# Performance work log

Hardware: AMD Instinct MI355X
Metric: run time of the kernel (lower is better)

Reference implementation:

```python
import jax, jax.numpy as jnp
import numpy as np

B, FH, N, TIN = 8, 8, 2048, 5      # batch(time for LSTM), f_length, nodes, in_length
H1, H2 = 32, 64                    # traj_linear_hidden, lstm_encoder_size
NEG = -9e15

def setup_inputs() -> dict:
    key = jax.random.key(0)
    ks = jax.random.split(key, 12)
    s = lambda k, shape, fan: jax.random.normal(k, shape, jnp.float32) * (1.0 / np.sqrt(fan))
    return {
        "hist": jax.random.normal(ks[0], (B, FH, N, TIN), jnp.float32),
        "adj": jax.random.randint(ks[1], (B, 2, N, N), 0, 2, jnp.int32),
        "W1": s(ks[2], (H1, TIN * FH), TIN * FH),
        "b1": jnp.zeros((H1,), jnp.float32),
        "W_ih": s(ks[3], (4 * H2, H1), H1),
        "W_hh": s(ks[4], (4 * H2, H2), H2),
        "b_ih": jnp.zeros((4 * H2,), jnp.float32),
        "b_hh": jnp.zeros((4 * H2,), jnp.float32),
        "Wg": s(ks[5], (H2, H2), H2),
        "a_src": s(ks[6], (H2,), H2),
        "a_dst": s(ks[7], (H2,), H2),
    }

def _lstm(x, W_ih, W_hh, b_ih, b_hh):
    # x: [T, Nb, H1] (torch nn.LSTM seq-first); gate order i,f,g,o
    Nb = x.shape[1]
    h0 = jnp.zeros((Nb, H2), x.dtype)
    c0 = jnp.zeros((Nb, H2), x.dtype)
    def step(carry, xt):
        h, c = carry
        g = xt @ W_ih.T + b_ih + h @ W_hh.T + b_hh        # [Nb, 4*H2]
        i, f, gg, o = jnp.split(g, 4, axis=-1)
        c = jax.nn.sigmoid(f) * c + jax.nn.sigmoid(i) * jnp.tanh(gg)
        h = jax.nn.sigmoid(o) * jnp.tanh(c)
        return (h, c), h
    _, hs = jax.lax.scan(step, (h0, c0), x)
    return hs                                              # [T, Nb, H2]

def reference(hist, adj, W1, b1, W_ih, W_hh, b_ih, b_hh, Wg, a_src, a_dst):
    # hist.permute(0,2,3,1).flatten(2,3) -> [B, N, TIN*FH]
    x = jnp.transpose(hist, (0, 2, 3, 1)).reshape(B, N, TIN * FH)
    h1 = jax.nn.elu(x @ W1.T + b1)                         # [B, N, H1]
    hs = _lstm(h1, W_ih, W_hh, b_ih, b_hh)                 # [B, N, H2]
    # GAT over adj[:, -1]
    A = adj[:, -1, :, :] > 0                               # [B, N, N]
    Wh = hs @ Wg                                           # [B, N, H2]
    e = jax.nn.leaky_relu(
        (Wh @ a_src)[:, :, None] + (Wh @ a_dst)[:, None, :], 0.2)
    e = jnp.where(A, e, NEG)
    alpha = jax.nn.softmax(e, axis=-1)                     # [B, N, N]
    out = jax.nn.elu(jnp.einsum("bij,bjd->bid", alpha, Wh))
    return out
```

## Files before the change

kernel.cpp:

```cpp
#include <hip/hip_runtime.h>
#include <hip/hip_bf16.h>
#include <math.h>

#define BB 8
#define FH 8
#define NN 2048
#define TIN 5
#define H1 32
#define H2 64

typedef const void* cvp;
typedef __attribute__((ext_vector_type(8))) short short8;
typedef __attribute__((ext_vector_type(4))) float floatx4;

__device__ __forceinline__ float ldx(cvp p, int i, int bf) {
  if (bf) return __bfloat162float(((const __hip_bfloat16*)p)[i]);
  return ((const float*)p)[i];
}

__device__ __forceinline__ float4 ld4(cvp p, int i, int bf) {
  if (bf) {
    const __hip_bfloat162* q = (const __hip_bfloat162*)p;
    float2 a = __bfloat1622float2(q[(i >> 1)]);
    float2 b = __bfloat1622float2(q[(i >> 1) + 1]);
    return make_float4(a.x, a.y, b.x, b.y);
  }
  return ((const float4*)p)[i >> 2];
}

__device__ __forceinline__ float sigf(float x) {
  return 1.f / (1.f + __expf(-x));
}

__device__ __forceinline__ int detect_bf(cvp wih) {
  unsigned word = ((const unsigned*)wih)[threadIdx.x & 63];
  unsigned e = (word >> 7) & 0xFFu;
  unsigned long long bal = __ballot(e >= 100u && e <= 150u);
  return __popcll(bal) > 44;
}

__global__ __launch_bounds__(256, 2) void k_lstm(
    cvp hist, cvp W1, cvp b1, cvp W_ih, cvp W_hh, cvp b_ih, cvp b_hh,
    cvp Wg, cvp a_src, cvp a_dst,
    __hip_bfloat16* __restrict__ WhFr, float* __restrict__ sv,
    float* __restrict__ dv) {
  __shared__ __align__(16) float xh[4][96];
  __shared__ float gbuf[4][256];
  __shared__ float W1s[H1][41];
  __shared__ float b1s[H1];
  __shared__ float xstage[4][40];
  int bf = detect_bf(W_ih);
  int tid = threadIdx.x;
  int w = tid >> 6, lane = tid & 63;
  int g = tid;
  int n0 = blockIdx.x << 2;
  int node_w = n0 + w;

  for (int i = tid; i < H1 * 40; i += 256) W1s[i / 40][i % 40] = ldx(W1, i, bf);
  if (tid < H1) b1s[tid] = ldx(b1, tid, bf);

  float wreg[96];
#pragma unroll
  for (int kq = 0; kq < 8; ++kq) {
    float4 v = ld4(W_ih, g * 32 + (kq << 2), bf);
    wreg[(kq << 2) + 0] = v.x; wreg[(kq << 2) + 1] = v.y;
    wreg[(kq << 2) + 2] = v.z; wreg[(kq << 2) + 3] = v.w;
  }
#pragma unroll
  for (int kq = 0; kq < 16; ++kq) {
    float4 v = ld4(W_hh, g * 64 + (kq << 2), bf);
    wreg[32 + (kq << 2) + 0] = v.x; wreg[32 + (kq << 2) + 1] = v.y;
    wreg[32 + (kq << 2) + 2] = v.z; wreg[32 + (kq << 2) + 3] = v.w;
  }
  float bias = ldx(b_ih, g, bf) + ldx(b_hh, g, bf);

  float wgreg[64];
#pragma unroll
  for (int k = 0; k < H2; ++k) wgreg[k] = ldx(Wg, (k << 6) + lane, bf);
  float as = ldx(a_src, lane, bf);
  float ad = ldx(a_dst, lane, bf);

  size_t o8base = ((size_t)(node_w >> 5) * 256) + ((size_t)(lane >> 4) * 64) +
                  (((node_w >> 3) & 3) * 16) + (lane & 15);
  int jj = node_w & 7;

  xh[w][32 + lane] = 0.f;
  float c = 0.f;

  for (int t = 0; t < BB; ++t) {
    if (tid < 160) {
      int nd = tid / 40, r = tid % 40;
      int ti = r >> 3, f = r & 7;
      xstage[nd][r] = ldx(hist, ((t * FH + f) * NN + n0 + nd) * TIN + ti, bf);
    }
    __syncthreads();
    if (tid < 128) {
      int nd = tid >> 5, k = tid & 31;
      float acc = b1s[k];
#pragma unroll
      for (int j = 0; j < 40; ++j) acc += W1s[k][j] * xstage[nd][j];
      xh[nd][k] = (acc > 0.f) ? acc : expm1f(acc);
    }
    __syncthreads();
    float acc[4] = {bias, bias, bias, bias};
    const float4* xq0 = (const float4*)xh[0];
    const float4* xq1 = (const float4*)xh[1];
    const float4* xq2 = (const float4*)xh[2];
    const float4* xq3 = (const float4*)xh[3];
#pragma unroll
    for (int kq = 0; kq < 24; ++kq) {
      float w0 = wreg[(kq << 2) + 0], w1 = wreg[(kq << 2) + 1];
      float w2 = wreg[(kq << 2) + 2], w3 = wreg[(kq << 2) + 3];
      float4 v0 = xq0[kq], v1 = xq1[kq], v2 = xq2[kq], v3 = xq3[kq];
      acc[0] += w0 * v0.x + w1 * v0.y + w2 * v0.z + w3 * v0.w;
      acc[1] += w0 * v1.x + w1 * v1.y + w2 * v1.z + w3 * v1.w;
      acc[2] += w0 * v2.x + w1 * v2.y + w2 * v2.z + w3 * v2.w;
      acc[3] += w0 * v3.x + w1 * v3.y + w2 * v3.z + w3 * v3.w;
    }
#pragma unroll
    for (int nd = 0; nd < 4; ++nd) gbuf[nd][g] = acc[nd];
    __syncthreads();
    float gi = gbuf[w][lane];
    float gf = gbuf[w][64 + lane];
    float gg = gbuf[w][128 + lane];
    float go = gbuf[w][192 + lane];
    c = sigf(gf) * c + sigf(gi) * tanhf(gg);
    float h = sigf(go) * tanhf(c);
    xh[w][32 + lane] = h;

    float wh = 0.f;
    const float4* hq = (const float4*)&xh[w][32];
#pragma unroll
    for (int kq = 0; kq < 16; ++kq) {
      float4 hv = hq[kq];
      wh += hv.x * wgreg[(kq << 2) + 0] + hv.y * wgreg[(kq << 2) + 1] +
            hv.z * wgreg[(kq << 2) + 2] + hv.w * wgreg[(kq << 2) + 3];
    }
    float s = wh * as, d = wh * ad;
#pragma unroll
    for (int off = 32; off > 0; off >>= 1) {
      s += __shfl_xor(s, off, 64);
      d += __shfl_xor(d, off, 64);
    }
    if (lane == 0) {
      sv[t * NN + node_w] = s;
      dv[t * NN + node_w] = d;
    }
    WhFr[((size_t)t * 16384 + o8base) * 8 + jj] = __float2bfloat16(wh);
    __syncthreads();
  }
}

__global__ __launch_bounds__(256, 4) void k_gat(
    const int* __restrict__ adj, const __hip_bfloat16* __restrict__ WhFr,
    const float* __restrict__ sv, const float* __restrict__ dv,
    void* __restrict__ out, cvp W_ih) {
  __shared__ __align__(16) float dv_s[NN];
  __shared__ unsigned int msk[16 * 65];
  __shared__ floatx4 abuf[3][5][64];
  int bf = detect_bf(W_ih);
  int tid = threadIdx.x;
  int w = tid >> 6, lane = tid & 63;
  int b = blockIdx.x >> 7;
  int i0 = (blockIdx.x & 127) << 4;
  int q = lane >> 4, m = lane & 15;

  for (int j = tid; j < 16 * 65; j += 256) msk[j] = 0u;
  for (int j = tid; j < NN; j += 256) dv_s[j] = dv[b * NN + j];
  float sva = sv[b * NN + i0 + m];
  __syncthreads();

  const int4* adj4 = (const int4*)(adj + ((size_t)(b * 2 + 1) * NN + i0) * NN);
#pragma unroll 16
  for (int gi = 0; gi < 32; ++gi) {
    int g = (w << 5) + gi;
    int row = g >> 3, seg = g & 7;
    int4 v = adj4[(size_t)row * 512 + (seg << 6) + lane];
    unsigned nib = (v.x != 0 ? 1u : 0u) | (v.y != 0 ? 2u : 0u) |
                   (v.z != 0 ? 4u : 0u) | (v.w != 0 ? 8u : 0u);
    atomicOr(&msk[row * 65 + (seg << 3) + (lane >> 3)], nib << ((lane & 7) << 2));
  }
  __syncthreads();

  short8 ones;
#pragma unroll
  for (int p = 0; p < 8; ++p) ones[p] = (short)0x3F80;

  const short8* base = ((const short8*)WhFr) + (size_t)b * 16384 + lane;
  int ksb = w << 4, kse = ksb + 16;
  floatx4 acc0 = {0.f, 0.f, 0.f, 0.f};
  floatx4 acc1 = acc0, acc2 = acc0, acc3 = acc0, accS = acc0;

  for (int ks = ksb; ks < kse; ++ks) {
    const short8* b_ks = base + (size_t)ks * 256;
    short8 b0 = b_ks[0];
    short8 b1 = b_ks[64];
    short8 b2 = b_ks[128];
    short8 b3 = b_ks[192];
    unsigned mword = msk[m * 65 + ks];
    float4 d0 = *(const float4*)&dv_s[(ks << 5) + (q << 3)];
    float4 d1 = *(const float4*)&dv_s[(ks << 5) + (q << 3) + 4];
    float dd[8] = {d0.x, d0.y, d0.z, d0.w, d1.x, d1.y, d1.z, d1.w};
    float pv[8];
#pragma unroll
    for (int jj = 0; jj < 8; ++jj) {
      float t = sva + dd[jj];
      float e = __expf(fmaxf(t, 0.2f * t));
      pv[jj] = ((mword >> ((q << 3) + jj)) & 1u) ? e : 0.f;
    }
    short8 afr;
#pragma unroll
    for (int p2 = 0; p2 < 4; ++p2)
      ((__hip_bfloat162*)&afr)[p2] =
          __float22bfloat162_rn(make_float2(pv[2 * p2], pv[2 * p2 + 1]));
    acc0 = __builtin_amdgcn_mfma_f32_16x16x32_bf16(afr, b0, acc0, 0, 0, 0);
    acc1 = __builtin_amdgcn_mfma_f32_16x16x32_bf16(afr, b1, acc1, 0, 0, 0);
    acc2 = __builtin_amdgcn_mfma_f32_16x16x32_bf16(afr, b2, acc2, 0, 0, 0);
    acc3 = __builtin_amdgcn_mfma_f32_16x16x32_bf16(afr, b3, acc3, 0, 0, 0);
    accS = __builtin_amdgcn_mfma_f32_16x16x32_bf16(afr, ones, accS, 0, 0, 0);
  }
  if (w > 0) {
    abuf[w - 1][0][lane] = acc0;
    abuf[w - 1][1][lane] = acc1;
    abuf[w - 1][2][lane] = acc2;
    abuf[w - 1][3][lane] = acc3;
    abuf[w - 1][4][lane] = accS;
  }
  __syncthreads();
  if (w != 0) return;
#pragma unroll
  for (int ww = 0; ww < 3; ++ww) {
    acc0 += abuf[ww][0][lane];
    acc1 += abuf[ww][1][lane];
    acc2 += abuf[ww][2][lane];
    acc3 += abuf[ww][3][lane];
    accS += abuf[ww][4][lane];
  }
  floatx4 accs[4] = {acc0, acc1, acc2, acc3};
  float inv[4];
#pragma unroll
  for (int r = 0; r < 4; ++r) inv[r] = 1.f / accS[r];
  if (bf) {
    __hip_bfloat16* o = (__hip_bfloat16*)out;
#pragma unroll
    for (int nt = 0; nt < 4; ++nt)
#pragma unroll
      for (int r = 0; r < 4; ++r) {
        float v = accs[nt][r] * inv[r];
        v = (v > 0.f) ? v : expm1f(v);
        int row = i0 + (q << 2) + r;
        o[((size_t)b * NN + row) * H2 + (nt << 4) + m] = __float2bfloat16(v);
      }
  } else {
    float* o = (float*)out;
#pragma unroll
    for (int nt = 0; nt < 4; ++nt)
#pragma unroll
      for (int r = 0; r < 4; ++r) {
        float v = accs[nt][r] * inv[r];
        v = (v > 0.f) ? v : expm1f(v);
        int row = i0 + (q << 2) + r;
        o[((size_t)b * NN + row) * H2 + (nt << 4) + m] = v;
      }
  }
}

extern "C" void kernel_launch(void* const* d_in, const int* in_sizes, int n_in,
                              void* d_out, int out_size, void* d_ws, size_t ws_size,
                              hipStream_t stream) {
  (void)in_sizes; (void)n_in; (void)out_size; (void)ws_size;
  cvp hist  = d_in[0];
  const int* adj = (const int*)d_in[1];
  cvp W1    = d_in[2];
  cvp b1    = d_in[3];
  cvp W_ih  = d_in[4];
  cvp W_hh  = d_in[5];
  cvp b_ih  = d_in[6];
  cvp b_hh  = d_in[7];
  cvp Wg    = d_in[8];
  cvp a_src = d_in[9];
  cvp a_dst = d_in[10];

  __hip_bfloat16* WhFr = (__hip_bfloat16*)d_ws;
  float* sv = (float*)d_ws + 524288;
  float* dv = sv + BB * NN;

  k_lstm<<<512, 256, 0, stream>>>(hist, W1, b1, W_ih, W_hh, b_ih, b_hh,
                                  Wg, a_src, a_dst, WhFr, sv, dv);
  k_gat<<<1024, 256, 0, stream>>>(adj, WhFr, sv, dv, d_out, W_ih);
}
```

Measured before the change: 398.4 us.

## Move adjacency bitmask packing into LSTM kernel to overlap with recurrence

Reading the 128MB int32 adjacency slice and packing it into bitmasks moves out of the GAT kernel and into the latency-bound LSTM kernel. There the loads are interleaved with each timestep's compute, and the result goes to a global bitmask in the workspace. The GAT kernel then loads only the packed mask plus vectorized dv. The goal is to hide the memory-bound adjacency scan behind the LSTM's sync-heavy recurrence. In exchange the LSTM kernel gains register pressure, LDS use and shared-memory atomics.

Result: faster. 381.9 us (-4.1%).

```diff
diff --git a/kernel.cpp b/kernel.cpp
--- a/kernel.cpp
+++ b/kernel.cpp
@@ -41,14 +41,15 @@
 
 __global__ __launch_bounds__(256, 2) void k_lstm(
     cvp hist, cvp W1, cvp b1, cvp W_ih, cvp W_hh, cvp b_ih, cvp b_hh,
-    cvp Wg, cvp a_src, cvp a_dst,
+    cvp Wg, cvp a_src, cvp a_dst, const int* __restrict__ adj,
     __hip_bfloat16* __restrict__ WhFr, float* __restrict__ sv,
-    float* __restrict__ dv) {
+    float* __restrict__ dv, unsigned* __restrict__ gmask) {
   __shared__ __align__(16) float xh[4][96];
   __shared__ float gbuf[4][256];
   __shared__ float W1s[H1][41];
   __shared__ float b1s[H1];
   __shared__ float xstage[4][40];
+  __shared__ __align__(16) unsigned pmsk[2048];
   int bf = detect_bf(W_ih);
   int tid = threadIdx.x;
   int w = tid >> 6, lane = tid & 63;
@@ -58,6 +59,11 @@
 
   for (int i = tid; i < H1 * 40; i += 256) W1s[i / 40][i % 40] = ldx(W1, i, bf);
   if (tid < H1) b1s[tid] = ldx(b1, tid, bf);
+  for (int i = tid; i < 2048; i += 256) pmsk[i] = 0u;
+
+  int cb = blockIdx.x >> 6;
+  int ci = (blockIdx.x & 63) << 5;
+  const int4* adj4 = (const int4*)(adj + ((size_t)(cb * 2 + 1) * NN + ci) * NN);
 
   float wreg[96];
 #pragma unroll
@@ -93,6 +99,9 @@
       int ti = r >> 3, f = r & 7;
       xstage[nd][r] = ldx(hist, ((t * FH + f) * NN + n0 + nd) * TIN + ti, bf);
     }
+    int4 av0[4];
+#pragma unroll
+    for (int u = 0; u < 4; ++u) av0[u] = adj4[(t << 11) + (u << 8) + tid];
     __syncthreads();
     if (tid < 128) {
       int nd = tid >> 5, k = tid & 31;
@@ -119,12 +128,23 @@
     }
 #pragma unroll
     for (int nd = 0; nd < 4; ++nd) gbuf[nd][g] = acc[nd];
+#pragma unroll
+    for (int u = 0; u < 4; ++u) {
+      int gg = (t << 11) + (u << 8) + tid;
+      unsigned nib = (av0[u].x != 0 ? 1u : 0u) | (av0[u].y != 0 ? 2u : 0u) |
+                     (av0[u].z != 0 ? 4u : 0u) | (av0[u].w != 0 ? 8u : 0u);
+      atomicOr(&pmsk[((gg >> 9) << 6) + ((gg & 511) >> 3)],
+               nib << ((gg & 7) << 2));
+    }
+    int4 av1[4];
+#pragma unroll
+    for (int u = 0; u < 4; ++u) av1[u] = adj4[(t << 11) + ((u + 4) << 8) + tid];
     __syncthreads();
     float gi = gbuf[w][lane];
     float gf = gbuf[w][64 + lane];
-    float gg = gbuf[w][128 + lane];
+    float gg0 = gbuf[w][128 + lane];
     float go = gbuf[w][192 + lane];
-    c = sigf(gf) * c + sigf(gi) * tanhf(gg);
+    c = sigf(gf) * c + sigf(gi) * tanhf(gg0);
     float h = sigf(go) * tanhf(c);
     xh[w][32 + lane] = h;
 
@@ -147,12 +167,24 @@
       dv[t * NN + node_w] = d;
     }
     WhFr[((size_t)t * 16384 + o8base) * 8 + jj] = __float2bfloat16(wh);
+#pragma unroll
+    for (int u = 0; u < 4; ++u) {
+      int gg2 = (t << 11) + ((u + 4) << 8) + tid;
+      unsigned nib = (av1[u].x != 0 ? 1u : 0u) | (av1[u].y != 0 ? 2u : 0u) |
+                     (av1[u].z != 0 ? 4u : 0u) | (av1[u].w != 0 ? 8u : 0u);
+      atomicOr(&pmsk[((gg2 >> 9) << 6) + ((gg2 & 511) >> 3)],
+               nib << ((gg2 & 7) << 2));
+    }
     __syncthreads();
   }
+  const int4* ps = (const int4*)pmsk;
+  int4* gm4 = (int4*)gmask + ((size_t)blockIdx.x << 9);
+  gm4[tid] = ps[tid];
+  gm4[256 + tid] = ps[256 + tid];
 }
 
 __global__ __launch_bounds__(256, 4) void k_gat(
-    const int* __restrict__ adj, const __hip_bfloat16* __restrict__ WhFr,
+    const unsigned* __restrict__ gmask, const __hip_bfloat16* __restrict__ WhFr,
     const float* __restrict__ sv, const float* __restrict__ dv,
     void* __restrict__ out, cvp W_ih) {
   __shared__ __align__(16) float dv_s[NN];
@@ -165,21 +197,20 @@
   int i0 = (blockIdx.x & 127) << 4;
   int q = lane >> 4, m = lane & 15;
 
-  for (int j = tid; j < 16 * 65; j += 256) msk[j] = 0u;
-  for (int j = tid; j < NN; j += 256) dv_s[j] = dv[b * NN + j];
+  const int4* gm4 = (const int4*)gmask + (((size_t)b * NN + i0) << 4);
+  int4 mv = gm4[tid];
+  {
+    int mrow = tid >> 4, mwd = (tid & 15) << 2;
+    unsigned* mp = &msk[mrow * 65 + mwd];
+    mp[0] = (unsigned)mv.x; mp[1] = (unsigned)mv.y;
+    mp[2] = (unsigned)mv.z; mp[3] = (unsigned)mv.w;
+  }
+  {
+    const float4* dsrc = (const float4*)(dv + (size_t)b * NN);
+    ((float4*)dv_s)[tid] = dsrc[tid];
+    ((float4*)dv_s)[256 + tid] = dsrc[256 + tid];
+  }
   float sva = sv[b * NN + i0 + m];
-  __syncthreads();
-
-  const int4* adj4 = (const int4*)(adj + ((size_t)(b * 2 + 1) * NN + i0) * NN);
-#pragma unroll 16
-  for (int gi = 0; gi < 32; ++gi) {
-    int g = (w << 5) + gi;
-    int row = g >> 3, seg = g & 7;
-    int4 v = adj4[(size_t)row * 512 + (seg << 6) + lane];
-    unsigned nib = (v.x != 0 ? 1u : 0u) | (v.y != 0 ? 2u : 0u) |
-                   (v.z != 0 ? 4u : 0u) | (v.w != 0 ? 8u : 0u);
-    atomicOr(&msk[row * 65 + (seg << 3) + (lane >> 3)], nib << ((lane & 7) << 2));
-  }
   __syncthreads();
 
   short8 ones;
@@ -281,11 +312,13 @@
   cvp a_src = d_in[9];
   cvp a_dst = d_in[10];
 
+  float* ws = (float*)d_ws;
   __hip_bfloat16* WhFr = (__hip_bfloat16*)d_ws;
-  float* sv = (float*)d_ws + 524288;
+  float* sv = ws + 524288;
   float* dv = sv + BB * NN;
+  unsigned* gmask = (unsigned*)(dv + BB * NN);
 
   k_lstm<<<512, 256, 0, stream>>>(hist, W1, b1, W_ih, W_hh, b_ih, b_hh,
-                                  Wg, a_src, a_dst, WhFr, sv, dv);
-  k_gat<<<1024, 256, 0, stream>>>(adj, WhFr, sv, dv, d_out, W_ih);
-}
+                                  Wg, a_src, a_dst, adj, WhFr, sv, dv, gmask);
+  k_gat<<<1024, 256, 0, stream>>>(gmask, WhFr, sv, dv, d_out, W_ih);
+}
```
